# Performance work log

Hardware: AMD Instinct MI355X
Metric: run time of the kernel (lower is better)

Reference implementation:

```python
import jax, jax.numpy as jnp
import numpy as np

N_NODES = 4096
N_EDGES = 524288
IN_DIM = 6
EMB_N = 4
EMB_D = 8
EDGE_D = 1
HID = 64
N_HEADS = 4
LN_EPS = 1e-5


def _layernorm(h, g, b):
    m = jnp.mean(h, axis=-1, keepdims=True)
    v = jnp.mean(jnp.square(h - m), axis=-1, keepdims=True)
    return (h - m) * jax.lax.rsqrt(v + LN_EPS) * g + b


def setup_inputs() -> dict:
    key = jax.random.key(0)
    ks = jax.random.split(key, 16)
    s = lambda fan_in: 1.0 / np.sqrt(fan_in)
    inp = {
        'x': jax.random.normal(ks[0], (N_NODES, IN_DIM), jnp.float32),
        'edge_attr': jax.random.uniform(ks[1], (N_EDGES, EDGE_D), jnp.float32),
        'entity_emb': jax.random.normal(ks[2], (EMB_N, EMB_D), jnp.float32),
        'lin1_w': jax.random.uniform(ks[3], (HID, IN_DIM + EMB_D + EDGE_D), jnp.float32, -s(15), s(15)),
        'lin1_b': jnp.zeros((HID,), jnp.float32),
        'lay_w': jax.random.uniform(ks[4], (HID, HID), jnp.float32, -s(HID), s(HID)),
        'lay_b': jnp.zeros((HID,), jnp.float32),
        'ln_g': jnp.ones((HID,), jnp.float32),
        'ln_b': jnp.zeros((HID,), jnp.float32),
        'in_proj_w': jax.random.uniform(ks[5], (3 * HID, HID), jnp.float32, -s(HID), s(HID)),
        'in_proj_b': jnp.zeros((3 * HID,), jnp.float32),
        'out_proj_w': jax.random.uniform(ks[6], (HID, HID), jnp.float32, -s(HID), s(HID)),
        'out_proj_b': jnp.zeros((HID,), jnp.float32),
        'an_g': jnp.ones((HID,), jnp.float32),
        'an_b': jnp.zeros((HID,), jnp.float32),
        'out_w': jax.random.uniform(ks[7], (HID, HID), jnp.float32, -s(HID), s(HID)),
        'out_b': jnp.zeros((HID,), jnp.float32),
        'edge_index': jax.random.randint(ks[8], (2, N_EDGES), 0, N_NODES, jnp.int64),
        'entity_type': jax.random.randint(ks[9], (N_NODES,), 0, EMB_N, jnp.int64),
    }
    return inp


def reference(x, edge_attr, entity_emb, lin1_w, lin1_b, lay_w, lay_b, ln_g, ln_b,
              in_proj_w, in_proj_b, out_proj_w, out_proj_b, an_g, an_b, out_w, out_b,
              edge_index, entity_type):
    # --- EmbedConv ---
    # concat node features with entity embedding: [N, 6+8]
    xe = jnp.concatenate([x, entity_emb[entity_type]], axis=-1)
    src, dst = edge_index[0], edge_index[1]
    # gather source nodes + edge attr: [E, 15]
    msg = jnp.concatenate([xe[src], edge_attr], axis=-1)
    msg = _layernorm(jax.nn.relu(msg @ lin1_w.T + lin1_b), ln_g, ln_b)
    # layer_N = 1 extra layer, shared LayerNorm
    msg = _layernorm(jax.nn.relu(msg @ lay_w.T + lay_b), ln_g, ln_b)
    # scatter-add aggregate into destination nodes: [N, 64]
    h = jax.ops.segment_sum(msg, dst, num_segments=N_NODES)
    # --- MultiheadAttention over all nodes as one sequence (eval: no dropout) ---
    qkv = h @ in_proj_w.T + in_proj_b  # [N, 3H]
    q, k, v = jnp.split(qkv, 3, axis=-1)
    hd = HID // N_HEADS
    q = q.reshape(N_NODES, N_HEADS, hd).transpose(1, 0, 2)  # [h, n, d]
    k = k.reshape(N_NODES, N_HEADS, hd).transpose(1, 0, 2)
    v = v.reshape(N_NODES, N_HEADS, hd).transpose(1, 0, 2)
    scores = jnp.einsum('hnd,hmd->hnm', q, k) / np.sqrt(hd)
    attn = jax.nn.softmax(scores, axis=-1)
    o = jnp.einsum('hnm,hmd->hnd', attn, v).transpose(1, 0, 2).reshape(N_NODES, HID)
    o = o @ out_proj_w.T + out_proj_b
    h = _layernorm(h + o, an_g, an_b)
    # --- output layer ---
    return h @ out_w.T + out_b
```

## Files before the change

### kernel.cpp

```cpp
#include <hip/hip_runtime.h>

#define N_NODES 4096
#define N_EDGES 524288
#define HID 64

typedef short short8 __attribute__((ext_vector_type(8)));
typedef float f32x4 __attribute__((ext_vector_type(4)));
typedef float f32x16 __attribute__((ext_vector_type(16)));

__device__ __forceinline__ float bcastf(float v, int l) {
    return __int_as_float(__builtin_amdgcn_readlane(__float_as_int(v), l));
}

__device__ __forceinline__ void wave_sum2(float& a, float& b) {
    #pragma unroll
    for (int off = 32; off > 0; off >>= 1) {
        a += __shfl_xor(a, off, 64);
        b += __shfl_xor(b, off, 64);
    }
}

__device__ __forceinline__ short f2bf(float f) {
    unsigned u = __float_as_uint(f);
    u = u + 0x7FFFu + ((u >> 16) & 1u);
    return (short)(u >> 16);
}
__device__ __forceinline__ float bf2f(short s) {
    return __uint_as_float(((unsigned)(unsigned short)s) << 16);
}
__device__ __forceinline__ void split_cheap(float f, short& hi, short& lo) {
    unsigned u = __float_as_uint(f);
    unsigned hb = u & 0xffff0000u;
    float lof = f - __uint_as_float(hb);
    hi = (short)(u >> 16);
    lo = (short)(__float_as_uint(lof) >> 16);
}

__device__ __forceinline__ void pack_plane8(const float* vv, short8& ah, short8& al) {
    union { unsigned u[4]; short8 s; } Uh, Ul;
    #pragma unroll
    for (int i = 0; i < 4; i++) {
        unsigned hw;
        asm("v_cvt_pk_bf16_f32 %0, %1, %2" : "=v"(hw) : "v"(vv[2 * i]), "v"(vv[2 * i + 1]));
        float he = __uint_as_float(hw << 16);
        float ho = __uint_as_float(hw & 0xffff0000u);
        float le = vv[2 * i] - he;
        float lo_ = vv[2 * i + 1] - ho;
        unsigned lw;
        asm("v_cvt_pk_bf16_f32 %0, %1, %2" : "=v"(lw) : "v"(le), "v"(lo_));
        Uh.u[i] = hw; Ul.u[i] = lw;
    }
    ah = Uh.s; al = Ul.s;
}

__device__ __forceinline__ void pack_pfrag(const float* p, short8& pf0s, short8& pf1s) {
    unsigned w0, w1, w2, w3, u0, u1, u2, u3;
    asm("v_cvt_pk_bf16_f32 %0, %1, %2" : "=v"(w0) : "v"(p[0]), "v"(p[1]));
    asm("v_cvt_pk_bf16_f32 %0, %1, %2" : "=v"(w1) : "v"(p[2]), "v"(p[3]));
    asm("v_cvt_pk_bf16_f32 %0, %1, %2" : "=v"(w2) : "v"(p[4]), "v"(p[5]));
    asm("v_cvt_pk_bf16_f32 %0, %1, %2" : "=v"(w3) : "v"(p[6]), "v"(p[7]));
    asm("v_cvt_pk_bf16_f32 %0, %1, %2" : "=v"(u0) : "v"(p[8]), "v"(p[9]));
    asm("v_cvt_pk_bf16_f32 %0, %1, %2" : "=v"(u1) : "v"(p[10]), "v"(p[11]));
    asm("v_cvt_pk_bf16_f32 %0, %1, %2" : "=v"(u2) : "v"(p[12]), "v"(p[13]));
    asm("v_cvt_pk_bf16_f32 %0, %1, %2" : "=v"(u3) : "v"(p[14]), "v"(p[15]));
    asm("v_permlane32_swap_b32 %0, %1" : "+v"(w0), "+v"(w2));
    asm("v_permlane32_swap_b32 %0, %1" : "+v"(w1), "+v"(w3));
    asm("v_permlane32_swap_b32 %0, %1" : "+v"(u0), "+v"(u2));
    asm("v_permlane32_swap_b32 %0, %1" : "+v"(u1), "+v"(u3));
    union { unsigned u[4]; short8 s; } pf0, pf1;
    pf0.u[0] = w0; pf0.u[1] = w1; pf0.u[2] = w2; pf0.u[3] = w3;
    pf1.u[0] = u0; pf1.u[1] = u1; pf1.u[2] = u2; pf1.u[3] = u3;
    pf0s = pf0.s; pf1s = pf1.s;
}

__global__ void hist_prep(const float* __restrict__ x, const float* __restrict__ emb,
                          const int* __restrict__ etype, const int* __restrict__ ei,
                          const float* __restrict__ w1, const float* __restrict__ b1,
                          const float* __restrict__ w2, const float* __restrict__ lng,
                          const float* __restrict__ lnb, const float* __restrict__ b2,
                          const float* __restrict__ ipw,
                          float* __restrict__ A1, int* __restrict__ cnt, int* __restrict__ rank,
                          unsigned short* __restrict__ w2fh, unsigned short* __restrict__ w2fl,
                          unsigned short* __restrict__ ipfh, unsigned short* __restrict__ ipfl,
                          float* __restrict__ b2p, float* __restrict__ w14p) {
    int tid = blockIdx.x * 256 + threadIdx.x;
    int d = ei[N_EDGES + tid];
    rank[tid] = atomicAdd(&cnt[d], 1);
    if (tid < N_NODES * 64) {
        int n = tid >> 6, f = tid & 63;
        const float* wr = w1 + f * 15;
        float acc = b1[f];
        #pragma unroll
        for (int k = 0; k < 6; k++) acc = fmaf(x[n * 6 + k], wr[k], acc);
        int e = etype[n];
        #pragma unroll
        for (int k = 0; k < 8; k++) acc = fmaf(emb[e * 8 + k], wr[6 + k], acc);
        A1[tid] = acc;
    }
    if (tid < 4096) {
        int idx = tid >> 9, ln = (tid >> 3) & 63, j = tid & 7;
        int mm = ln & 15, qq = ln >> 4;
        int g = idx >> 1, tt = idx & 1;
        int col = tt * 32 + qq * 8 + j;
        float w = w2[(g * 16 + mm) * 64 + col] * lng[col];
        short hi = f2bf(w);
        w2fh[tid] = (unsigned short)hi;
        w2fl[tid] = (unsigned short)f2bf(w - bf2f(hi));
    }
    if (tid < 12288) {
        int idx = tid >> 9, ln = (tid >> 3) & 63, j = tid & 7;
        int mm = ln & 15, qq = ln >> 4;
        int og = idx >> 1, tt = idx & 1;
        float w = ipw[(og * 16 + mm) * 64 + tt * 32 + qq * 8 + j];
        short hi = f2bf(w);
        ipfh[tid] = (unsigned short)hi;
        ipfl[tid] = (unsigned short)f2bf(w - bf2f(hi));
    }
    if (tid < 64) {
        float acc = b2[tid];
        for (int c = 0; c < 64; c++) acc = fmaf(w2[tid * 64 + c], lnb[c], acc);
        b2p[tid] = acc;
        w14p[tid] = w1[tid * 15 + 14];
    }
}

__global__ void __launch_bounds__(256) scatter_scan(
        const int* __restrict__ cnt, const int* __restrict__ ei,
        const float* __restrict__ edge_attr, const int* __restrict__ rank,
        int* __restrict__ bnd,
        int* __restrict__ ssrc, float* __restrict__ sea) {
    __shared__ int lbnd[4096];
    __shared__ int wsum[4];
    int t = threadIdx.x;
    int base = t * 16;
    int v16[16];
    int T = 0;
    #pragma unroll
    for (int j4 = 0; j4 < 4; j4++) {
        int4 c4 = ((const int4*)cnt)[t * 4 + j4];
        v16[j4 * 4 + 0] = c4.x; v16[j4 * 4 + 1] = c4.y;
        v16[j4 * 4 + 2] = c4.z; v16[j4 * 4 + 3] = c4.w;
        T += c4.x + c4.y + c4.z + c4.w;
    }
    int inc = T;
    int l = t & 63;
    #pragma unroll
    for (int off = 1; off < 64; off <<= 1) {
        int v = __shfl_up(inc, off, 64);
        if (l >= off) inc += v;
    }
    if (l == 63) wsum[t >> 6] = inc;
    __syncthreads();
    int wo = 0;
    for (int w = 0; w < (t >> 6); w++) wo += wsum[w];
    int run = wo + inc - T;
    #pragma unroll
    for (int j = 0; j < 16; j++) {
        lbnd[base + j] = run;
        run += v16[j];
    }
    if (blockIdx.x == 0) {
        #pragma unroll
        for (int j = 0; j < 16; j++) bnd[base + j] = lbnd[base + j];
        if (t == 255) bnd[4096] = run;
    }
    __syncthreads();
    int e = blockIdx.x * 256 + t;
    int d = ei[N_EDGES + e];
    int pos = lbnd[d] + rank[e];
    ssrc[pos] = ei[e];
    sea[pos] = edge_attr[e];
}

__global__ void __launch_bounds__(256, 3) edge_gather_mfma(
        const float* __restrict__ A1,
        const int* __restrict__ ssrc, const float* __restrict__ sea,
        const int* __restrict__ bnd,
        const unsigned short* __restrict__ w2fh, const unsigned short* __restrict__ w2fl,
        const float* __restrict__ w14p, const float* __restrict__ b2p,
        const float* __restrict__ lg, const float* __restrict__ lb,
        float* __restrict__ h) {
    __shared__ uint4 lw2h4[512];
    __shared__ uint4 lw2l4[512];
    int tid = threadIdx.x;
    {
        const uint4* gh = (const uint4*)w2fh;
        const uint4* gl = (const uint4*)w2fl;
        lw2h4[tid] = gh[tid];
        lw2h4[tid + 256] = gh[tid + 256];
        lw2l4[tid] = gl[tid];
        lw2l4[tid + 256] = gl[tid + 256];
    }
    const unsigned short* lw2h = (const unsigned short*)lw2h4;
    const unsigned short* lw2l = (const unsigned short*)lw2l4;

    int lane = tid & 63;
    int wv = tid >> 6;
    int m = lane & 15;
    int q = lane >> 4;

    float w14f[16];
    {
        float4 wa = *(const float4*)(w14p + q * 8);
        float4 wb = *(const float4*)(w14p + q * 8 + 4);
        float4 wc = *(const float4*)(w14p + 32 + q * 8);
        float4 wd = *(const float4*)(w14p + 32 + q * 8 + 4);
        w14f[0] = wa.x; w14f[1] = wa.y; w14f[2] = wa.z; w14f[3] = wa.w;
        w14f[4] = wb.x; w14f[5] = wb.y; w14f[6] = wb.z; w14f[7] = wb.w;
        w14f[8] = wc.x; w14f[9] = wc.y; w14f[10] = wc.z; w14f[11] = wc.w;
        w14f[12] = wd.x; w14f[13] = wd.y; w14f[14] = wd.z; w14f[15] = wd.w;
    }
    float b2v[16];
    #pragma unroll
    for (int g = 0; g < 4; g++) {
        float4 bb = *(const float4*)(b2p + g * 16 + q * 4);
        b2v[g * 4 + 0] = bb.x; b2v[g * 4 + 1] = bb.y;
        b2v[g * 4 + 2] = bb.z; b2v[g * 4 + 3] = bb.w;
    }
    __syncthreads();

    int node = blockIdx.x * 4 + wv;
    int start = bnd[node], end = bnd[node + 1];
    int ntiles = (end - start + 15) >> 4;
    float acc[16];
    #pragma unroll
    for (int i = 0; i < 16; i++) acc[i] = 0.f;

    if (ntiles > 0) {
        int ec0 = start + m; if (ec0 >= end) ec0 = end - 1;
        int srcn0 = ssrc[ec0]; float eav0 = sea[ec0];
        int srcn1 = srcn0; float eav1 = eav0;
        if (ntiles > 1) {
            int ec1 = start + 16 + m; if (ec1 >= end) ec1 = end - 1;
            srcn1 = ssrc[ec1]; eav1 = sea[ec1];
        }
        const float* ar = A1 + srcn0 * 64 + q * 8;
        float4 va = *(const float4*)(ar);
        float4 vb = *(const float4*)(ar + 4);
        float4 vc = *(const float4*)(ar + 32);
        float4 vd = *(const float4*)(ar + 36);

        for (int t = 0; t < ntiles; t++) {
            int base = start + t * 16;
            const float* arn = A1 + srcn1 * 64 + q * 8;
            float4 na = *(const float4*)(arn);
            float4 nb = *(const float4*)(arn + 4);
            float4 nc = *(const float4*)(arn + 32);
            float4 nd = *(const float4*)(arn + 36);
            int srcn2 = srcn1; float eav2 = eav1;
            if (t + 2 < ntiles) {
                int ec2 = base + 32 + m; if (ec2 >= end) ec2 = end - 1;
                srcn2 = ssrc[ec2]; eav2 = sea[ec2];
            }
            float v[16] = {va.x, va.y, va.z, va.w, vb.x, vb.y, vb.z, vb.w,
                           vc.x, vc.y, vc.z, vc.w, vd.x, vd.y, vd.z, vd.w};
            float eavc = eav0;
            float s = 0.f, s2 = 0.f;
            #pragma unroll
            for (int j = 0; j < 16; j++) {
                float u = fmaxf(fmaf(w14f[j], eavc, v[j]), 0.f);
                v[j] = u;
                s += u;
                s2 = fmaf(u, u, s2);
            }
            s += __shfl_xor(s, 16, 64);  s2 += __shfl_xor(s2, 16, 64);
            s += __shfl_xor(s, 32, 64);  s2 += __shfl_xor(s2, 32, 64);
            float mean = s * (1.f / 64.f);
            float var = s2 * (1.f / 64.f) - mean * mean;
            float rs = rsqrtf(var + 1e-5f);
            float a0 = -mean * rs;
            #pragma unroll
            for (int j = 0; j < 16; j++) v[j] = fmaf(v[j], rs, a0);
            short8 a2h[2], a2l[2];
            pack_plane8(v, a2h[0], a2l[0]);
            pack_plane8(v + 8, a2h[1], a2l[1]);
            int ob = (t >> 20);
            float s_ = 0.f, s2_ = 0.f;
            float t2v[16];
            #pragma unroll
            for (int g = 0; g < 4; g++) {
                f32x4 c = {0.f, 0.f, 0.f, 0.f};
                #pragma unroll
                for (int t2 = 0; t2 < 2; t2++) {
                    short8 bh = *(const short8*)(lw2h + ((g * 2 + t2) * 64 + lane + ob) * 8);
                    short8 bl = *(const short8*)(lw2l + ((g * 2 + t2) * 64 + lane + ob) * 8);
                    c = __builtin_amdgcn_mfma_f32_16x16x32_bf16(bh, a2l[t2], c, 0, 0, 0);
                    c = __builtin_amdgcn_mfma_f32_16x16x32_bf16(bl, a2h[t2], c, 0, 0, 0);
                    c = __builtin_amdgcn_mfma_f32_16x16x32_bf16(bh, a2h[t2], c, 0, 0, 0);
                }
                #pragma unroll
                for (int r = 0; r < 4; r++) {
                    float vv = fmaxf(c[r] + b2v[g * 4 + r], 0.f);
                    t2v[g * 4 + r] = vv;
                    s_ += vv;
                    s2_ = fmaf(vv, vv, s2_);
                }
            }
            s_ += __shfl_xor(s_, 16, 64);  s2_ += __shfl_xor(s2_, 16, 64);
            s_ += __shfl_xor(s_, 32, 64);  s2_ += __shfl_xor(s2_, 32, 64);
            float mean2 = s_ * (1.f / 64.f);
            float var2 = s2_ * (1.f / 64.f) - mean2 * mean2;
            float rs2 = rsqrtf(var2 + 1e-5f);
            float a02 = -mean2 * rs2;
            if (base + m < end) {
                #pragma unroll
                for (int i = 0; i < 16; i++) acc[i] += fmaf(t2v[i], rs2, a02);
            }
            va = na; vb = nb; vc = nc; vd = nd;
            eav0 = eav1; eav1 = eav2; srcn1 = srcn2;
        }
    }
    #pragma unroll
    for (int off = 1; off < 16; off <<= 1)
        #pragma unroll
        for (int i = 0; i < 16; i++) acc[i] += __shfl_xor(acc[i], off, 64);
    if (m == 0) {
        float deg = (float)(end - start);
        #pragma unroll
        for (int g = 0; g < 4; g++) {
            float4 lgv = *(const float4*)(lg + g * 16 + q * 4);
            float4 lbv = *(const float4*)(lb + g * 16 + q * 4);
            float* hp = h + node * 64 + g * 16 + q * 4;
            hp[0] = lgv.x * acc[g * 4 + 0] + deg * lbv.x;
            hp[1] = lgv.y * acc[g * 4 + 1] + deg * lbv.y;
            hp[2] = lgv.z * acc[g * 4 + 2] + deg * lbv.z;
            hp[3] = lgv.w * acc[g * 4 + 3] + deg * lbv.w;
        }
    }
}

__global__ void __launch_bounds__(256) qkv_mfma(
        const float* __restrict__ h, const float* __restrict__ b,
        const unsigned short* __restrict__ ipfh, const unsigned short* __restrict__ ipfl,
        unsigned short* __restrict__ qhp, unsigned short* __restrict__ qlp,
        unsigned short* __restrict__ khp, unsigned short* __restrict__ klp,
        unsigned short* __restrict__ vT) {
    int lane = threadIdx.x & 63;
    int wv = threadIdx.x >> 6;
    int m = lane & 15;
    int q = lane >> 4;
    int wid = blockIdx.x * 4 + wv;
    int tile = wid / 12;
    int og = wid - tile * 12;
    short8 bh[2], bl[2];
    #pragma unroll
    for (int t = 0; t < 2; t++) {
        bh[t] = *(const short8*)(ipfh + ((og * 2 + t) * 64 + lane) * 8);
        bl[t] = *(const short8*)(ipfl + ((og * 2 + t) * 64 + lane) * 8);
    }
    f32x4 c = {0.f, 0.f, 0.f, 0.f};
    #pragma unroll
    for (int t = 0; t < 2; t++) {
        const float* hr = h + (tile * 16 + m) * 64 + t * 32 + q * 8;
        float4 f0 = *(const float4*)hr;
        float4 f1 = *(const float4*)(hr + 4);
        float av8[8] = {f0.x, f0.y, f0.z, f0.w, f1.x, f1.y, f1.z, f1.w};
        short8 ah, al;
        #pragma unroll
        for (int j = 0; j < 8; j++) {
            short hi, lo;
            split_cheap(av8[j], hi, lo);
            ah[j] = hi;
            al[j] = lo;
        }
        c = __builtin_amdgcn_mfma_f32_16x16x32_bf16(al, bh[t], c, 0, 0, 0);
        c = __builtin_amdgcn_mfma_f32_16x16x32_bf16(ah, bl[t], c, 0, 0, 0);
        c = __builtin_amdgcn_mfma_f32_16x16x32_bf16(ah, bh[t], c, 0, 0, 0);
    }
    int o = og * 16 + m;
    float bias = b[o];
    #pragma unroll
    for (int r = 0; r < 4; r++) {
        int node = tile * 16 + q * 4 + r;
        float val = c[r] + bias;
        if (og < 4) {
            float aq = val * (0.25f * 1.44269504f);
            size_t idx = ((size_t)(og * N_NODES + node)) * 16 + m;
            short hi = f2bf(aq);
            qhp[idx] = (unsigned short)hi;
            qlp[idx] = (unsigned short)f2bf(aq - bf2f(hi));
        } else if (og < 8) {
            size_t idx = ((size_t)((og - 4) * N_NODES + node)) * 16 + m;
            short hi = f2bf(val);
            khp[idx] = (unsigned short)hi;
            klp[idx] = (unsigned short)f2bf(val - bf2f(hi));
        } else {
            int feat = (og - 8) * 16 + m;
            vT[(size_t)feat * N_NODES + node] = (unsigned short)f2bf(val);
        }
    }
}

__global__ void __launch_bounds__(256) attn_mfma(
        const unsigned short* __restrict__ qhp, const unsigned short* __restrict__ qlp,
        const unsigned short* __restrict__ khp, const unsigned short* __restrict__ klp,
        const unsigned short* __restrict__ vT,
        float* __restrict__ part_o, float* __restrict__ part_ml) {
    int lane = threadIdx.x & 63;
    int wv = threadIdx.x >> 6;
    int l31 = lane & 31;
    int hi = lane >> 5;
    const short8 vones = {0x3F80, 0x3F80, 0x3F80, 0x3F80, 0x3F80, 0x3F80, 0x3F80, 0x3F80};

    int wid = blockIdx.x * 4 + wv;
    int kc = wid & 7;
    int wqt = (wid >> 3) & 127;
    int head = wid >> 10;

    int qrow = wqt * 32 + l31;
    short8 aqh = *(const short8*)(qhp + ((size_t)(head * N_NODES + qrow)) * 16 + hi * 8);
    short8 aql = *(const short8*)(qlp + ((size_t)(head * N_NODES + qrow)) * 16 + hi * 8);

    const unsigned short* khb = khp + (size_t)head * N_NODES * 16;
    const unsigned short* klb = klp + (size_t)head * N_NODES * 16;
    const unsigned short* vtb = vT + (size_t)(head * 16 + (l31 & 15)) * N_NODES;

    float mS = -3e38f;
    f32x16 Ot = {0.f, 0.f, 0.f, 0.f, 0.f, 0.f, 0.f, 0.f,
                 0.f, 0.f, 0.f, 0.f, 0.f, 0.f, 0.f, 0.f};

    for (int it = 0; it < 8; it++) {
        int n0 = kc * 512 + it * 64;
        size_t ka = ((size_t)(n0 + l31)) * 16 + hi * 8;
        size_t kb = ka + 32 * 16;
        short8 kah = *(const short8*)(khb + ka);
        short8 kal = *(const short8*)(klb + ka);
        short8 kbh = *(const short8*)(khb + kb);
        short8 kbl = *(const short8*)(klb + kb);
        f32x16 SA = {0.f, 0.f, 0.f, 0.f, 0.f, 0.f, 0.f, 0.f,
                     0.f, 0.f, 0.f, 0.f, 0.f, 0.f, 0.f, 0.f};
        f32x16 SB = SA;
        SA = __builtin_amdgcn_mfma_f32_32x32x16_bf16(kah, aql, SA, 0, 0, 0);
        SB = __builtin_amdgcn_mfma_f32_32x32x16_bf16(kbh, aql, SB, 0, 0, 0);
        SA = __builtin_amdgcn_mfma_f32_32x32x16_bf16(kal, aqh, SA, 0, 0, 0);
        SB = __builtin_amdgcn_mfma_f32_32x32x16_bf16(kbl, aqh, SB, 0, 0, 0);
        SA = __builtin_amdgcn_mfma_f32_32x32x16_bf16(kah, aqh, SA, 0, 0, 0);
        SB = __builtin_amdgcn_mfma_f32_32x32x16_bf16(kbh, aqh, SB, 0, 0, 0);
        float t0[8];
        #pragma unroll
        for (int r = 0; r < 8; r++)
            t0[r] = fmaxf(fmaxf(SA[r], SA[r + 8]), fmaxf(SB[r], SB[r + 8]));
        t0[0] = fmaxf(t0[0], t0[4]); t0[1] = fmaxf(t0[1], t0[5]);
        t0[2] = fmaxf(t0[2], t0[6]); t0[3] = fmaxf(t0[3], t0[7]);
        t0[0] = fmaxf(t0[0], t0[2]); t0[1] = fmaxf(t0[1], t0[3]);
        float mr = fmaxf(t0[0], t0[1]);
        mr = fmaxf(mr, __shfl_xor(mr, 32, 64));
        if (!__all(mr <= mS)) {
            float mn = fmaxf(mS, mr);
            float alpha = exp2f(mS - mn);
            mS = mn;
            #pragma unroll
            for (int r = 0; r < 9; r++) Ot[r] *= alpha;
        }
        #pragma unroll
        for (int r = 0; r < 16; r++) SA[r] = exp2f(SA[r] - mS);
        #pragma unroll
        for (int r = 0; r < 16; r++) SB[r] = exp2f(SB[r] - mS);
        {
            float p[16];
            #pragma unroll
            for (int r = 0; r < 16; r++) p[r] = SA[r];
            short8 pf0, pf1;
            pack_pfrag(p, pf0, pf1);
            short8 v0, v1;
            if (l31 < 16) {
                v0 = *(const short8*)(vtb + n0 + hi * 8);
                v1 = *(const short8*)(vtb + n0 + 16 + hi * 8);
            } else if (l31 == 16) {
                v0 = vones; v1 = vones;
            } else {
                v0 = (short8)0; v1 = (short8)0;
            }
            Ot = __builtin_amdgcn_mfma_f32_32x32x16_bf16(v0, pf0, Ot, 0, 0, 0);
            Ot = __builtin_amdgcn_mfma_f32_32x32x16_bf16(v1, pf1, Ot, 0, 0, 0);
        }
        {
            float p[16];
            #pragma unroll
            for (int r = 0; r < 16; r++) p[r] = SB[r];
            short8 pf0, pf1;
            pack_pfrag(p, pf0, pf1);
            short8 v0, v1;
            if (l31 < 16) {
                v0 = *(const short8*)(vtb + n0 + 32 + hi * 8);
                v1 = *(const short8*)(vtb + n0 + 48 + hi * 8);
            } else if (l31 == 16) {
                v0 = vones; v1 = vones;
            } else {
                v0 = (short8)0; v1 = (short8)0;
            }
            Ot = __builtin_amdgcn_mfma_f32_32x32x16_bf16(v0, pf0, Ot, 0, 0, 0);
            Ot = __builtin_amdgcn_mfma_f32_32x32x16_bf16(v1, pf1, Ot, 0, 0, 0);
        }
    }
    int qt16 = wqt * 2 + (l31 >> 4);
    int qi = l31 & 15;
    size_t pb = ((size_t)(head * 8 + kc) * 256 + qt16) * 256;
    f32x4 o0 = {Ot[0], Ot[1], Ot[2], Ot[3]};
    f32x4 o1 = {Ot[4], Ot[5], Ot[6], Ot[7]};
    *(f32x4*)(part_o + pb + qi * 16 + hi * 4) = o0;
    *(f32x4*)(part_o + pb + qi * 16 + 8 + hi * 4) = o1;
    if (lane < 32) {
        size_t mb = ((size_t)(head * 8 + kc) * 256 + qt16) * 32;
        part_ml[mb + qi] = mS;
        part_ml[mb + 16 + qi] = Ot[8];
    }
}

__global__ void post_kernel(const float* __restrict__ h,
                            const float* __restrict__ part_o, const float* __restrict__ part_ml,
                            const float* __restrict__ opw, const float* __restrict__ opb,
                            const float* __restrict__ ag, const float* __restrict__ ab,
                            const float* __restrict__ ow, const float* __restrict__ ob,
                            float* __restrict__ out) {
    __shared__ float wl1[64 * 65];
    __shared__ float wl2[64 * 65];
    for (int i = threadIdx.x; i < 4096; i += blockDim.x) {
        int r = i >> 6, c = i & 63;
        wl1[r * 65 + c] = opw[i];
        wl2[r * 65 + c] = ow[i];
    }
    __syncthreads();
    int lane = threadIdx.x & 63;
    int n = blockIdx.x * 4 + (threadIdx.x >> 6);
    int j = lane;
    int head = j >> 4, d = j & 15;
    int qt = n >> 4, qi = n & 15;
    float M = -3e38f, L = 0.f, Ov = 0.f;
    #pragma unroll
    for (int c = 0; c < 8; c++) {
        size_t base = ((size_t)(head * 8 + c) * 256 + qt);
        float mc = part_ml[base * 32 + qi];
        float lc = part_ml[base * 32 + 16 + qi];
        float ov = part_o[base * 256 + qi * 16 + d];
        if (mc > M) {
            float sc = exp2f(M - mc);
            M = mc;
            L = L * sc + lc;
            Ov = Ov * sc + ov;
        } else {
            float sc = exp2f(mc - M);
            L = fmaf(lc, sc, L);
            Ov = fmaf(ov, sc, Ov);
        }
    }
    float oj = Ov / L;
    float acc = opb[j];
    #pragma unroll
    for (int k = 0; k < 64; k++) acc = fmaf(wl1[j * 65 + k], bcastf(oj, k), acc);
    float r = h[n * 64 + j] + acc;
    float s = r, s2 = r * r;
    wave_sum2(s, s2);
    float mean = s * (1.f / 64.f);
    float var = s2 * (1.f / 64.f) - mean * mean;
    float hn = (r - mean) * rsqrtf(var + 1e-5f) * ag[j] + ab[j];
    float acc2 = ob[j];
    #pragma unroll
    for (int k = 0; k < 64; k++) acc2 = fmaf(wl2[j * 65 + k], bcastf(hn, k), acc2);
    out[n * 64 + j] = acc2;
}

extern "C" void kernel_launch(void* const* d_in, const int* in_sizes, int n_in,
                              void* d_out, int out_size, void* d_ws, size_t ws_size,
                              hipStream_t stream) {
    const float* x        = (const float*)d_in[0];
    const float* edge_attr= (const float*)d_in[1];
    const float* emb      = (const float*)d_in[2];
    const float* lin1_w   = (const float*)d_in[3];
    const float* lin1_b   = (const float*)d_in[4];
    const float* lay_w    = (const float*)d_in[5];
    const float* lay_b    = (const float*)d_in[6];
    const float* ln_g     = (const float*)d_in[7];
    const float* ln_b     = (const float*)d_in[8];
    const float* ipw      = (const float*)d_in[9];
    const float* ipb      = (const float*)d_in[10];
    const float* opw      = (const float*)d_in[11];
    const float* opb      = (const float*)d_in[12];
    const float* ang      = (const float*)d_in[13];
    const float* anb      = (const float*)d_in[14];
    const float* ow       = (const float*)d_in[15];
    const float* ob       = (const float*)d_in[16];
    const int*   ei       = (const int*)d_in[17];
    const int*   et       = (const int*)d_in[18];

    char* wsb = (char*)d_ws;
    size_t off = 0;
    float* A1             = (float*)(wsb + off);          off += 1048576;
    float* h              = (float*)(wsb + off);          off += 1048576;
    unsigned short* qhp   = (unsigned short*)(wsb + off); off += 524288;
    unsigned short* qlp   = (unsigned short*)(wsb + off); off += 524288;
    unsigned short* khp   = (unsigned short*)(wsb + off); off += 524288;
    unsigned short* klp   = (unsigned short*)(wsb + off); off += 524288;
    unsigned short* vT    = (unsigned short*)(wsb + off); off += 524288;
    float* part_o         = (float*)(wsb + off);          off += 8388608;
    float* part_ml        = (float*)(wsb + off);          off += 1048576;
    int*   cnt            = (int*)(wsb + off);            off += 16384;
    int*   bnd            = (int*)(wsb + off);            off += 16388;
    off = (off + 255) & ~(size_t)255;
    int*   rank           = (int*)(wsb + off);            off += 2097152;
    int*   ssrc           = (int*)(wsb + off);            off += 2097152;
    float* sea            = (float*)(wsb + off);          off += 2097152;
    unsigned short* w2fh  = (unsigned short*)(wsb + off); off += 8192;
    unsigned short* w2fl  = (unsigned short*)(wsb + off); off += 8192;
    unsigned short* ipfh  = (unsigned short*)(wsb + off); off += 24576;
    unsigned short* ipfl  = (unsigned short*)(wsb + off); off += 24576;
    float* b2p            = (float*)(wsb + off);          off += 256;
    float* w14p           = (float*)(wsb + off);          off += 256;

    (void)hipMemsetAsync(cnt, 0, 4096 * sizeof(int), stream);
    hist_prep<<<2048, 256, 0, stream>>>(x, emb, et, ei, lin1_w, lin1_b, lay_w, ln_g, ln_b,
                                        lay_b, ipw, A1, cnt, rank, w2fh, w2fl, ipfh, ipfl,
                                        b2p, w14p);
    scatter_scan<<<2048, 256, 0, stream>>>(cnt, ei, edge_attr, rank, bnd, ssrc, sea);
    edge_gather_mfma<<<1024, 256, 0, stream>>>(A1, ssrc, sea, bnd, w2fh, w2fl,
                                               w14p, b2p, ln_g, ln_b, h);
    qkv_mfma<<<768, 256, 0, stream>>>(h, ipb, ipfh, ipfl, qhp, qlp, khp, klp, vT);
    attn_mfma<<<1024, 256, 0, stream>>>(qhp, qlp, khp, klp, vT, part_o, part_ml);
    post_kernel<<<1024, 256, 0, stream>>>(h, part_o, part_ml, opw, opb, ang, anb, ow, ob,
                                          (float*)d_out);
}
```

Baseline: 221.6 us.

## Pad V layout with ones row, prefetch K and V loads in attention loop

Measured after the change: 219.1 us. No clear change (-1.1%).

```diff
diff --git a/kernel.cpp b/kernel.cpp
--- a/kernel.cpp
+++ b/kernel.cpp
@@ -82,7 +82,8 @@
                           float* __restrict__ A1, int* __restrict__ cnt, int* __restrict__ rank,
                           unsigned short* __restrict__ w2fh, unsigned short* __restrict__ w2fl,
                           unsigned short* __restrict__ ipfh, unsigned short* __restrict__ ipfl,
-                          float* __restrict__ b2p, float* __restrict__ w14p) {
+                          float* __restrict__ b2p, float* __restrict__ w14p,
+                          unsigned short* __restrict__ vT) {
     int tid = blockIdx.x * 256 + threadIdx.x;
     int d = ei[N_EDGES + tid];
     rank[tid] = atomicAdd(&cnt[d], 1);
@@ -96,6 +97,13 @@
         #pragma unroll
         for (int k = 0; k < 8; k++) acc = fmaf(emb[e * 8 + k], wr[6 + k], acc);
         A1[tid] = acc;
+    }
+    if (tid < 262144) {
+        int vh = tid >> 16;
+        int rem = tid & 65535;
+        int dd = rem >> 12;
+        int nd = rem & 4095;
+        vT[((size_t)(vh * 32 + 16 + dd)) * N_NODES + nd] = (dd == 0) ? 0x3F80 : 0;
     }
     if (tid < 4096) {
         int idx = tid >> 9, ln = (tid >> 3) & 63, j = tid & 7;
@@ -385,13 +393,12 @@
             khp[idx] = (unsigned short)hi;
             klp[idx] = (unsigned short)f2bf(val - bf2f(hi));
         } else {
-            int feat = (og - 8) * 16 + m;
-            vT[(size_t)feat * N_NODES + node] = (unsigned short)f2bf(val);
-        }
-    }
-}
-
-__global__ void __launch_bounds__(256) attn_mfma(
+            vT[((size_t)((og - 8) * 32 + m)) * N_NODES + node] = (unsigned short)f2bf(val);
+        }
+    }
+}
+
+__global__ void __launch_bounds__(256, 4) attn_mfma(
         const unsigned short* __restrict__ qhp, const unsigned short* __restrict__ qlp,
         const unsigned short* __restrict__ khp, const unsigned short* __restrict__ klp,
         const unsigned short* __restrict__ vT,
@@ -400,7 +407,6 @@
     int wv = threadIdx.x >> 6;
     int l31 = lane & 31;
     int hi = lane >> 5;
-    const short8 vones = {0x3F80, 0x3F80, 0x3F80, 0x3F80, 0x3F80, 0x3F80, 0x3F80, 0x3F80};
 
     int wid = blockIdx.x * 4 + wv;
     int kc = wid & 7;
@@ -413,20 +419,30 @@
 
     const unsigned short* khb = khp + (size_t)head * N_NODES * 16;
     const unsigned short* klb = klp + (size_t)head * N_NODES * 16;
-    const unsigned short* vtb = vT + (size_t)(head * 16 + (l31 & 15)) * N_NODES;
+    const unsigned short* vtb = vT + (size_t)(head * 32 + l31) * N_NODES;
 
     float mS = -3e38f;
     f32x16 Ot = {0.f, 0.f, 0.f, 0.f, 0.f, 0.f, 0.f, 0.f,
                  0.f, 0.f, 0.f, 0.f, 0.f, 0.f, 0.f, 0.f};
 
+    size_t k0 = ((size_t)(kc * 512 + l31)) * 16 + hi * 8;
+    short8 kah = *(const short8*)(khb + k0);
+    short8 kal = *(const short8*)(klb + k0);
+    short8 kbh = *(const short8*)(khb + k0 + 512);
+    short8 kbl = *(const short8*)(klb + k0 + 512);
+
     for (int it = 0; it < 8; it++) {
         int n0 = kc * 512 + it * 64;
-        size_t ka = ((size_t)(n0 + l31)) * 16 + hi * 8;
-        size_t kb = ka + 32 * 16;
-        short8 kah = *(const short8*)(khb + ka);
-        short8 kal = *(const short8*)(klb + ka);
-        short8 kbh = *(const short8*)(khb + kb);
-        short8 kbl = *(const short8*)(klb + kb);
+        int itn = (it + 1 < 8) ? (it + 1) : 7;
+        size_t kn = ((size_t)(kc * 512 + itn * 64 + l31)) * 16 + hi * 8;
+        short8 nkah = *(const short8*)(khb + kn);
+        short8 nkal = *(const short8*)(klb + kn);
+        short8 nkbh = *(const short8*)(khb + kn + 512);
+        short8 nkbl = *(const short8*)(klb + kn + 512);
+        short8 v0a = *(const short8*)(vtb + n0 + hi * 8);
+        short8 v1a = *(const short8*)(vtb + n0 + 16 + hi * 8);
+        short8 v0b = *(const short8*)(vtb + n0 + 32 + hi * 8);
+        short8 v1b = *(const short8*)(vtb + n0 + 48 + hi * 8);
         f32x16 SA = {0.f, 0.f, 0.f, 0.f, 0.f, 0.f, 0.f, 0.f,
                      0.f, 0.f, 0.f, 0.f, 0.f, 0.f, 0.f, 0.f};
         f32x16 SB = SA;
@@ -462,17 +478,8 @@
             for (int r = 0; r < 16; r++) p[r] = SA[r];
             short8 pf0, pf1;
             pack_pfrag(p, pf0, pf1);
-            short8 v0, v1;
-            if (l31 < 16) {
-                v0 = *(const short8*)(vtb + n0 + hi * 8);
-                v1 = *(const short8*)(vtb + n0 + 16 + hi * 8);
-            } else if (l31 == 16) {
-                v0 = vones; v1 = vones;
-            } else {
-                v0 = (short8)0; v1 = (short8)0;
-            }
-            Ot = __builtin_amdgcn_mfma_f32_32x32x16_bf16(v0, pf0, Ot, 0, 0, 0);
-            Ot = __builtin_amdgcn_mfma_f32_32x32x16_bf16(v1, pf1, Ot, 0, 0, 0);
+            Ot = __builtin_amdgcn_mfma_f32_32x32x16_bf16(v0a, pf0, Ot, 0, 0, 0);
+            Ot = __builtin_amdgcn_mfma_f32_32x32x16_bf16(v1a, pf1, Ot, 0, 0, 0);
         }
         {
             float p[16];
@@ -480,18 +487,10 @@
             for (int r = 0; r < 16; r++) p[r] = SB[r];
             short8 pf0, pf1;
             pack_pfrag(p, pf0, pf1);
-            short8 v0, v1;
-            if (l31 < 16) {
-                v0 = *(const short8*)(vtb + n0 + 32 + hi * 8);
-                v1 = *(const short8*)(vtb + n0 + 48 + hi * 8);
-            } else if (l31 == 16) {
-                v0 = vones; v1 = vones;
-            } else {
-                v0 = (short8)0; v1 = (short8)0;
-            }
-            Ot = __builtin_amdgcn_mfma_f32_32x32x16_bf16(v0, pf0, Ot, 0, 0, 0);
-            Ot = __builtin_amdgcn_mfma_f32_32x32x16_bf16(v1, pf1, Ot, 0, 0, 0);
-        }
+            Ot = __builtin_amdgcn_mfma_f32_32x32x16_bf16(v0b, pf0, Ot, 0, 0, 0);
+            Ot = __builtin_amdgcn_mfma_f32_32x32x16_bf16(v1b, pf1, Ot, 0, 0, 0);
+        }
+        kah = nkah; kal = nkal; kbh = nkbh; kbl = nkbl;
     }
     int qt16 = wqt * 2 + (l31 >> 4);
     int qi = l31 & 15;
@@ -591,7 +590,7 @@
     unsigned short* qlp   = (unsigned short*)(wsb + off); off += 524288;
     unsigned short* khp   = (unsigned short*)(wsb + off); off += 524288;
     unsigned short* klp   = (unsigned short*)(wsb + off); off += 524288;
-    unsigned short* vT    = (unsigned short*)(wsb + off); off += 524288;
+    unsigned short* vT    = (unsigned short*)(wsb + off); off += 1048576;
     float* part_o         = (float*)(wsb + off);          off += 8388608;
     float* part_ml        = (float*)(wsb + off);          off += 1048576;
     int*   cnt            = (int*)(wsb + off);            off += 16384;
@@ -610,7 +609,7 @@
     (void)hipMemsetAsync(cnt, 0, 4096 * sizeof(int), stream);
     hist_prep<<<2048, 256, 0, stream>>>(x, emb, et, ei, lin1_w, lin1_b, lay_w, ln_g, ln_b,
                                         lay_b, ipw, A1, cnt, rank, w2fh, w2fl, ipfh, ipfl,
-                                        b2p, w14p);
+                                        b2p, w14p, vT);
     scatter_scan<<<2048, 256, 0, stream>>>(cnt, ei, edge_attr, rank, bnd, ssrc, sea);
     edge_gather_mfma<<<1024, 256, 0, stream>>>(A1, ssrc, sea, bnd, w2fh, w2fl,
                                                w14p, b2p, ln_g, ln_b, h);
```
